# Performance work log

Measured on AMD Instinct MI355X. Metric: run time of the kernel, lower is better.

Reference implementation:

```python
import jax, jax.numpy as jnp
import numpy as np

B, L, R = 4, 2048, 1024        # batch, seq_len, residual_dim
HID, EXP, K = 64, 2, 3          # hidden_dim, expansion_factor, conv_kernel_size
D = HID * EXP                   # ssm_input_dim = 128
N = HID                         # SSM state size = 64


def setup_inputs() -> dict:
    key = jax.random.key(0)
    ks = jax.random.split(key, 16)
    g = lambda k, s: jax.random.normal(k, s, dtype=jnp.float32) * 0.02
    inp = {
        "up_x":   jax.random.normal(ks[0], (B, L, R), dtype=jnp.float32),
        "W_up":   g(ks[1], (R, 2 * D)),
        "b_up":   g(ks[2], (2 * D,)),
        "conv_w": g(ks[3], (D, K)),          # depthwise Conv1d weight [C,1,K] squeezed
        "conv_b": g(ks[4], (D,)),
        "W_delta": g(ks[5], (D, D)),
        "b_delta": g(ks[6], (D,)),
        "W_B":    g(ks[7], (D, N)),
        "b_B":    g(ks[8], (N,)),
        "W_C":    g(ks[9], (D, N)),
        "b_C":    g(ks[10], (N,)),
        "A_log":  jnp.log(jnp.broadcast_to(jnp.arange(1, N + 1, dtype=jnp.float32), (D, N))),
        "D_skip": jnp.ones((D,), dtype=jnp.float32),
        "W_down": g(ks[11], (D, R)),
        "b_down": g(ks[12], (R,)),
    }
    return inp


def reference(up_x, W_up, b_up, conv_w, conv_b, W_delta, b_delta,
              W_B, b_B, W_C, b_C, A_log, D_skip, W_down, b_down):
    Lq = up_x.shape[1]
    u = up_x @ W_up + b_up                               # [B,L,2D]
    left, right = jnp.split(u, 2, axis=-1)               # each [B,L,D]

    # causal depthwise conv (pad left K-1, truncate to L)
    xp = jnp.pad(left, ((0, 0), (K - 1, 0), (0, 0)))     # [B,L+K-1,D]
    conv = sum(conv_w[:, k] * xp[:, k:k + Lq, :] for k in range(K)) + conv_b
    x = jax.nn.silu(conv)                                # [B,L,D]

    # S6 selective scan
    delta = jax.nn.softplus(x @ W_delta + b_delta)       # [B,L,D]
    Bm = x @ W_B + b_B                                   # [B,L,N]
    Cm = x @ W_C + b_C                                   # [B,L,N]
    A = -jnp.exp(A_log)                                  # [D,N]
    dA = jnp.exp(delta[..., None] * A)                   # [B,L,D,N]
    dBx = delta[..., None] * Bm[:, :, None, :] * x[..., None]  # [B,L,D,N]

    def step(h, inputs):
        dA_t, dBx_t, C_t = inputs                        # [B,D,N],[B,D,N],[B,N]
        h = dA_t * h + dBx_t
        y_t = jnp.einsum('bdn,bn->bd', h, C_t)
        return h, y_t

    h0 = jnp.zeros((up_x.shape[0], D, N), dtype=x.dtype)
    _, ys = jax.lax.scan(step, h0, (jnp.swapaxes(dA, 0, 1),
                                    jnp.swapaxes(dBx, 0, 1),
                                    jnp.swapaxes(Cm, 0, 1)))
    y = jnp.swapaxes(ys, 0, 1) + D_skip * x              # [B,L,D]

    gated = y * jax.nn.silu(right)                       # SiLU gate
    return gated @ W_down + b_down                       # [B,L,R]
```

## Files before the change

### kernel.cpp

```cpp
#include <hip/hip_runtime.h>
#include <math.h>

#define B_ 4
#define L_ 2048
#define R_ 1024
#define D_ 128
#define N_ 64
#define TWO_D 256
#define M_ (B_*L_)

#define LNC 5
#define NC 32

#define LSTR 68
#define LSTRX 136

typedef __attribute__((ext_vector_type(8))) short bf16x8;
typedef __attribute__((ext_vector_type(4))) float f32x4;
typedef __attribute__((ext_vector_type(4))) unsigned short u16x4;

__device__ __forceinline__ float silu_f(float z) {
    return z * __builtin_amdgcn_rcpf(1.0f + __expf(-z));
}

__device__ __forceinline__ float softplus_f(float z) {
    return fmaxf(z, 0.0f) + __logf(1.0f + __expf(-fabsf(z)));
}

__device__ __forceinline__ short f2bf(float f) {
    union { float f; unsigned int u; } v; v.f = f;
    unsigned int r = v.u + 0x7FFF + ((v.u >> 16) & 1);
    return (short)(r >> 16);
}

__device__ __forceinline__ float bf2f(unsigned short s) {
    union { float f; unsigned int u; } v;
    v.u = ((unsigned int)s) << 16;
    return v.f;
}

__device__ __forceinline__ bf16x8 pack8(float4 a, float4 b) {
    bf16x8 r;
    r[0] = f2bf(a.x); r[1] = f2bf(a.y); r[2] = f2bf(a.z); r[3] = f2bf(a.w);
    r[4] = f2bf(b.x); r[5] = f2bf(b.y); r[6] = f2bf(b.z); r[7] = f2bf(b.w);
    return r;
}

__global__ __launch_bounds__(256) void gemm_up_splitk(
    const float* __restrict__ A,
    const float* __restrict__ W,
    float* __restrict__ P0,
    float* __restrict__ P1)
{
    __shared__ short Al[128 * LSTR];
    __shared__ short Bl[64 * LSTR];

    int lid = blockIdx.x;
    int xcd = lid & 7;
    int slot = lid >> 3;
    int bm = xcd * 8 + (slot >> 3);
    int r3 = slot & 7;
    int bn = r3 & 3;
    int split = r3 >> 2;
    float* P = split ? P1 : P0;
    int k0 = split * 512;

    int tid = threadIdx.x;
    int w = tid >> 6, l = tid & 63;
    int lm = l & 15, q = l >> 4;
    int wm = w * 32;

    f32x4 acc[2][4];
    #pragma unroll
    for (int i = 0; i < 2; i++)
        #pragma unroll
        for (int f = 0; f < 4; f++)
            acc[i][f] = (f32x4){0.f, 0.f, 0.f, 0.f};

    int ar = tid >> 1, ak = (tid & 1) * 16;
    int bcol = tid & 63, bk = (tid >> 6) * 8;

    const float* Ag = A + (size_t)(bm * 128 + ar) * 1024 + k0 + ak;
    const float* Wg = W + (size_t)k0 * TWO_D + (size_t)bn * 64 + bcol;

    for (int kt = 0; kt < 512; kt += 32) {
        float4 a0 = *(const float4*)(Ag + kt);
        float4 a1 = *(const float4*)(Ag + kt + 4);
        float4 a2 = *(const float4*)(Ag + kt + 8);
        float4 a3 = *(const float4*)(Ag + kt + 12);
        *(bf16x8*)&Al[ar * LSTR + ak]     = pack8(a0, a1);
        *(bf16x8*)&Al[ar * LSTR + ak + 8] = pack8(a2, a3);

        float w0 = Wg[(size_t)(kt + bk + 0) * TWO_D];
        float w1 = Wg[(size_t)(kt + bk + 1) * TWO_D];
        float w2 = Wg[(size_t)(kt + bk + 2) * TWO_D];
        float w3 = Wg[(size_t)(kt + bk + 3) * TWO_D];
        float w4 = Wg[(size_t)(kt + bk + 4) * TWO_D];
        float w5 = Wg[(size_t)(kt + bk + 5) * TWO_D];
        float w6 = Wg[(size_t)(kt + bk + 6) * TWO_D];
        float w7 = Wg[(size_t)(kt + bk + 7) * TWO_D];
        *(bf16x8*)&Bl[bcol * LSTR + bk] =
            pack8(make_float4(w0, w1, w2, w3), make_float4(w4, w5, w6, w7));

        __syncthreads();

        bf16x8 af0 = *(bf16x8*)&Al[(wm + lm) * LSTR + q * 8];
        bf16x8 af1 = *(bf16x8*)&Al[(wm + 16 + lm) * LSTR + q * 8];
        bf16x8 bfr[4];
        #pragma unroll
        for (int f = 0; f < 4; f++)
            bfr[f] = *(bf16x8*)&Bl[(f * 16 + lm) * LSTR + q * 8];

        #pragma unroll
        for (int f = 0; f < 4; f++) {
            acc[0][f] = __builtin_amdgcn_mfma_f32_16x16x32_bf16(af0, bfr[f], acc[0][f], 0, 0, 0);
            acc[1][f] = __builtin_amdgcn_mfma_f32_16x16x32_bf16(af1, bfr[f], acc[1][f], 0, 0, 0);
        }

        __syncthreads();
    }

    #pragma unroll
    for (int i = 0; i < 2; i++)
        #pragma unroll
        for (int f = 0; f < 4; f++)
            #pragma unroll
            for (int e = 0; e < 4; e++) {
                int row = bm * 128 + wm + i * 16 + q * 4 + e;
                int col = bn * 64 + f * 16 + lm;
                P[(size_t)row * TWO_D + col] = acc[i][f][e];
            }
}

__global__ __launch_bounds__(256) void convproj_mfma(
    const float* __restrict__ P0,
    const float* __restrict__ P1,
    const float* __restrict__ b_up,
    const float* __restrict__ conv_w,
    const float* __restrict__ conv_b,
    const float* __restrict__ W_delta, const float* __restrict__ b_delta,
    const float* __restrict__ W_B,     const float* __restrict__ b_B,
    const float* __restrict__ W_C,     const float* __restrict__ b_C,
    unsigned short* __restrict__ x,
    float* __restrict__ u,
    unsigned short* __restrict__ delta,
    unsigned short* __restrict__ Bm,
    unsigned short* __restrict__ Cm)
{
    __shared__ float uu[66 * 128];
    __shared__ short Xl[64 * LSTRX];
    __shared__ short Bl[64 * LSTR];

    int lid = blockIdx.x;
    int xcd = lid & 7;
    int slot = lid >> 3;
    int bm = xcd * 16 + (slot >> 2);
    int bn = slot & 3;
    int tid = threadIdx.x;

    bool seq_start = (bm & 31) == 0;

    #pragma unroll
    for (int i = 0; i < 9; i++) {
        int fi = tid + i * 256;
        if (fi < 2112) {
            int row = fi >> 5;
            int c4 = (fi & 31) * 4;
            int gr = bm * 64 + row - 2;
            float4 v;
            if (seq_start && row < 2) {
                v = make_float4(0.f, 0.f, 0.f, 0.f);
            } else {
                size_t gi = (size_t)gr * TWO_D + c4;
                float4 p0 = *(const float4*)&P0[gi];
                float4 p1 = *(const float4*)&P1[gi];
                float4 bb = *(const float4*)&b_up[c4];
                v = make_float4(p0.x + p1.x + bb.x, p0.y + p1.y + bb.y,
                                p0.z + p1.z + bb.z, p0.w + p1.w + bb.w);
            }
            *(float4*)&uu[fi * 4] = v;
        }
    }

    if (bn == 1) {
        #pragma unroll
        for (int i = 0; i < 8; i++) {
            int fi = tid + i * 256;
            int row = fi >> 5;
            int c4 = (fi & 31) * 4 + 128;
            int gr = bm * 64 + row;
            size_t gi = (size_t)gr * TWO_D + c4;
            float4 p0 = *(const float4*)&P0[gi];
            float4 p1 = *(const float4*)&P1[gi];
            float4 bb = *(const float4*)&b_up[c4];
            *(float4*)&u[gi] = make_float4(p0.x + p1.x + bb.x, p0.y + p1.y + bb.y,
                                           p0.z + p1.z + bb.z, p0.w + p1.w + bb.w);
        }
    }
    __syncthreads();

    #pragma unroll
    for (int i = 0; i < 8; i++) {
        int fi = tid + i * 256;
        int row = fi >> 5;
        int c4 = (fi & 31) * 4;
        float4 v2 = *(const float4*)&uu[(row + 2) * 128 + c4];
        float4 v1 = *(const float4*)&uu[(row + 1) * 128 + c4];
        float4 v0 = *(const float4*)&uu[(row + 0) * 128 + c4];
        float4 z;
        {
            float w0 = conv_w[(c4 + 0) * 3 + 0], w1 = conv_w[(c4 + 0) * 3 + 1], w2 = conv_w[(c4 + 0) * 3 + 2];
            z.x = silu_f(fmaf(w0, v0.x, fmaf(w1, v1.x, fmaf(w2, v2.x, conv_b[c4 + 0]))));
        }
        {
            float w0 = conv_w[(c4 + 1) * 3 + 0], w1 = conv_w[(c4 + 1) * 3 + 1], w2 = conv_w[(c4 + 1) * 3 + 2];
            z.y = silu_f(fmaf(w0, v0.y, fmaf(w1, v1.y, fmaf(w2, v2.y, conv_b[c4 + 1]))));
        }
        {
            float w0 = conv_w[(c4 + 2) * 3 + 0], w1 = conv_w[(c4 + 2) * 3 + 1], w2 = conv_w[(c4 + 2) * 3 + 2];
            z.z = silu_f(fmaf(w0, v0.z, fmaf(w1, v1.z, fmaf(w2, v2.z, conv_b[c4 + 2]))));
        }
        {
            float w0 = conv_w[(c4 + 3) * 3 + 0], w1 = conv_w[(c4 + 3) * 3 + 1], w2 = conv_w[(c4 + 3) * 3 + 2];
            z.w = silu_f(fmaf(w0, v0.w, fmaf(w1, v1.w, fmaf(w2, v2.w, conv_b[c4 + 3]))));
        }
        short4 zb;
        zb.x = f2bf(z.x); zb.y = f2bf(z.y); zb.z = f2bf(z.z); zb.w = f2bf(z.w);
        *(short4*)&Xl[row * LSTRX + c4] = zb;
        if (bn == 0) {
            int gr = bm * 64 + row;
            *(short4*)&x[(size_t)gr * D_ + c4] = zb;
        }
    }

    const float* Wsel; const float* bsel; int wstride;
    if (bn < 2)       { Wsel = W_delta + bn * 64; bsel = b_delta + bn * 64; wstride = 128; }
    else if (bn == 2) { Wsel = W_B;               bsel = b_B;               wstride = 64;  }
    else              { Wsel = W_C;               bsel = b_C;               wstride = 64;  }

    int w = tid >> 6, l = tid & 63;
    int lm = l & 15, q = l >> 4;
    int wm = (w & 1) * 32, wn = (w >> 1) * 32;

    f32x4 acc00 = {0,0,0,0}, acc01 = {0,0,0,0}, acc10 = {0,0,0,0}, acc11 = {0,0,0,0};

    int bcol = tid & 63, bk = (tid >> 6) * 8;
    const float* Wg = Wsel + bcol;

    __syncthreads();

    for (int kt = 0; kt < 128; kt += 32) {
        float w0 = Wg[(size_t)(kt + bk + 0) * wstride];
        float w1 = Wg[(size_t)(kt + bk + 1) * wstride];
        float w2 = Wg[(size_t)(kt + bk + 2) * wstride];
        float w3 = Wg[(size_t)(kt + bk + 3) * wstride];
        float w4 = Wg[(size_t)(kt + bk + 4) * wstride];
        float w5 = Wg[(size_t)(kt + bk + 5) * wstride];
        float w6 = Wg[(size_t)(kt + bk + 6) * wstride];
        float w7 = Wg[(size_t)(kt + bk + 7) * wstride];
        *(bf16x8*)&Bl[bcol * LSTR + bk] =
            pack8(make_float4(w0, w1, w2, w3), make_float4(w4, w5, w6, w7));

        __syncthreads();

        bf16x8 af0 = *(bf16x8*)&Xl[(wm + lm) * LSTRX + kt + q * 8];
        bf16x8 af1 = *(bf16x8*)&Xl[(wm + 16 + lm) * LSTRX + kt + q * 8];
        bf16x8 bf0 = *(bf16x8*)&Bl[(wn + lm) * LSTR + q * 8];
        bf16x8 bf1 = *(bf16x8*)&Bl[(wn + 16 + lm) * LSTR + q * 8];

        acc00 = __builtin_amdgcn_mfma_f32_16x16x32_bf16(af0, bf0, acc00, 0, 0, 0);
        acc01 = __builtin_amdgcn_mfma_f32_16x16x32_bf16(af0, bf1, acc01, 0, 0, 0);
        acc10 = __builtin_amdgcn_mfma_f32_16x16x32_bf16(af1, bf0, acc10, 0, 0, 0);
        acc11 = __builtin_amdgcn_mfma_f32_16x16x32_bf16(af1, bf1, acc11, 0, 0, 0);

        __syncthreads();
    }

    #pragma unroll
    for (int i = 0; i < 4; i++) {
        int r0 = bm * 64 + wm + q * 4 + i;
        int r1 = r0 + 16;
        int c0 = wn + lm;
        int c1 = c0 + 16;
        float v00 = acc00[i] + bsel[c0];
        float v01 = acc01[i] + bsel[c1];
        float v10 = acc10[i] + bsel[c0];
        float v11 = acc11[i] + bsel[c1];
        if (bn < 2) {
            int cc0 = bn * 64 + c0, cc1 = bn * 64 + c1;
            delta[(size_t)r0 * D_ + cc0] = (unsigned short)f2bf(softplus_f(v00));
            delta[(size_t)r0 * D_ + cc1] = (unsigned short)f2bf(softplus_f(v01));
            delta[(size_t)r1 * D_ + cc0] = (unsigned short)f2bf(softplus_f(v10));
            delta[(size_t)r1 * D_ + cc1] = (unsigned short)f2bf(softplus_f(v11));
        } else if (bn == 2) {
            Bm[(size_t)r0 * N_ + c0] = (unsigned short)f2bf(v00);
            Bm[(size_t)r0 * N_ + c1] = (unsigned short)f2bf(v01);
            Bm[(size_t)r1 * N_ + c0] = (unsigned short)f2bf(v10);
            Bm[(size_t)r1 * N_ + c1] = (unsigned short)f2bf(v11);
        } else {
            Cm[(size_t)r0 * N_ + c0] = (unsigned short)f2bf(v00);
            Cm[(size_t)r0 * N_ + c1] = (unsigned short)f2bf(v01);
            Cm[(size_t)r1 * N_ + c0] = (unsigned short)f2bf(v10);
            Cm[(size_t)r1 * N_ + c1] = (unsigned short)f2bf(v11);
        }
    }
}

__global__ __launch_bounds__(256) void scan_sumA(
    const unsigned short* __restrict__ delta,
    const unsigned short* __restrict__ x,
    const unsigned short* __restrict__ Bm,
    const float* __restrict__ A_log,
    float* __restrict__ ch_aprod,
    float* __restrict__ ch_h)
{
    constexpr int TCt = L_ >> LNC;

    int blk = blockIdx.x;
    int c = blk & (NC - 1);
    int dqg = (blk >> LNC) & 7;
    int b = blk >> (LNC + 3);
    int wv = threadIdx.x >> 6;
    int l = threadIdx.x & 63;
    int g = l >> 4, j = l & 15;
    int dq = dqg * 4 + wv;
    int d = dq * 4 + g;

    const float LOG2E = 1.44269504089f;
    float4 Ar = *(const float4*)&A_log[d * N_ + j * 4];
    float Ai0 = -__expf(Ar.x) * LOG2E;
    float Ai1 = -__expf(Ar.y) * LOG2E;
    float Ai2 = -__expf(Ar.z) * LOG2E;
    float Ai3 = -__expf(Ar.w) * LOG2E;

    size_t row0 = (size_t)b * L_ + c * TCt;
    const unsigned short* dp = delta + row0 * D_ + d;
    const unsigned short* xp = x     + row0 * D_ + d;
    const unsigned short* bp = Bm    + row0 * N_ + j * 4;

    float h0 = 0, h1 = 0, h2 = 0, h3 = 0;
    float S = 0;

    #pragma unroll 8
    for (int t = 0; t < TCt; t++) {
        float dl = bf2f(dp[t * D_]);
        float xv = bf2f(xp[t * D_]);
        u16x4 bv = *(const u16x4*)&bp[t * N_];
        float e0 = exp2f(dl * Ai0);
        float e1 = exp2f(dl * Ai1);
        float e2 = exp2f(dl * Ai2);
        float e3 = exp2f(dl * Ai3);
        float dbx = dl * xv;
        h0 = fmaf(e0, h0, dbx * bf2f(bv[0]));
        h1 = fmaf(e1, h1, dbx * bf2f(bv[1]));
        h2 = fmaf(e2, h2, dbx * bf2f(bv[2]));
        h3 = fmaf(e3, h3, dbx * bf2f(bv[3]));
        S += dl;
    }

    size_t ci = (((size_t)b * D_ + d) * NC + c) * N_ + j * 4;
    *(float4*)&ch_aprod[ci] = make_float4(exp2f(Ai0 * S), exp2f(Ai1 * S),
                                          exp2f(Ai2 * S), exp2f(Ai3 * S));
    *(float4*)&ch_h[ci]     = make_float4(h0, h1, h2, h3);
}

__global__ __launch_bounds__(64) void scan_prefix(
    float* __restrict__ aprod_hin,
    const float* __restrict__ ch_h)
{
    int idx = blockIdx.x * 64 + threadIdx.x;
    int n = idx & 63;
    int rest = idx >> 6;
    size_t base = (size_t)rest * NC * N_ + n;
    float h = 0.0f;
    #pragma unroll 8
    for (int c = 0; c < NC; c++) {
        size_t o = base + (size_t)c * N_;
        float a  = aprod_hin[o];
        float hh = ch_h[o];
        aprod_hin[o] = h;
        h = fmaf(a, h, hh);
    }
}

__global__ __launch_bounds__(256) void scan_outB(
    const unsigned short* __restrict__ delta,
    const unsigned short* __restrict__ x,
    const unsigned short* __restrict__ Bm,
    const unsigned short* __restrict__ Cm,
    const float* __restrict__ A_log,
    const float* __restrict__ D_skip,
    const float* __restrict__ hin,
    const float* __restrict__ u,
    short* __restrict__ gated)
{
    constexpr int TCt = L_ >> LNC;
    __shared__ float yl[TCt * 16];

    int blk = blockIdx.x;
    int c = blk & (NC - 1);
    int dqg = (blk >> LNC) & 7;
    int b = blk >> (LNC + 3);
    int wv = threadIdx.x >> 6;
    int l = threadIdx.x & 63;
    int g = l >> 4, j = l & 15;
    int dq = dqg * 4 + wv;
    int d = dq * 4 + g;

    const float LOG2E = 1.44269504089f;
    float4 Ar = *(const float4*)&A_log[d * N_ + j * 4];
    float Ai0 = -__expf(Ar.x) * LOG2E;
    float Ai1 = -__expf(Ar.y) * LOG2E;
    float Ai2 = -__expf(Ar.z) * LOG2E;
    float Ai3 = -__expf(Ar.w) * LOG2E;
    float dsk = D_skip[d];

    float4 hv = *(const float4*)&hin[(((size_t)b * D_ + d) * NC + c) * N_ + j * 4];
    float h0 = hv.x, h1 = hv.y, h2 = hv.z, h3 = hv.w;

    size_t row0 = (size_t)b * L_ + c * TCt;
    const unsigned short* dp = delta + row0 * D_ + d;
    const unsigned short* xp = x     + row0 * D_ + d;
    const unsigned short* bp = Bm    + row0 * N_ + j * 4;
    const unsigned short* cp = Cm    + row0 * N_ + j * 4;

    #pragma unroll 8
    for (int t = 0; t < TCt; t++) {
        float dl = bf2f(dp[t * D_]);
        float xv = bf2f(xp[t * D_]);
        u16x4 bv = *(const u16x4*)&bp[t * N_];
        u16x4 cv = *(const u16x4*)&cp[t * N_];
        float e0 = exp2f(dl * Ai0);
        float e1 = exp2f(dl * Ai1);
        float e2 = exp2f(dl * Ai2);
        float e3 = exp2f(dl * Ai3);
        float dbx = dl * xv;
        h0 = fmaf(e0, h0, dbx * bf2f(bv[0]));
        h1 = fmaf(e1, h1, dbx * bf2f(bv[1]));
        h2 = fmaf(e2, h2, dbx * bf2f(bv[2]));
        h3 = fmaf(e3, h3, dbx * bf2f(bv[3]));
        float p = fmaf(h0, bf2f(cv[0]), fmaf(h1, bf2f(cv[1]),
                  fmaf(h2, bf2f(cv[2]), h3 * bf2f(cv[3]))));
        p += __shfl_xor(p, 1, 64);
        p += __shfl_xor(p, 2, 64);
        p += __shfl_xor(p, 4, 64);
        p += __shfl_xor(p, 8, 64);
        if (j == 0) yl[t * 16 + wv * 4 + g] = fmaf(dsk, xv, p);
    }

    __syncthreads();

    int tid = threadIdx.x;
    {
        int t = tid >> 2;
        int c4 = (tid & 3) * 4;
        size_t row = row0 + t;
        float4 yv = *(float4*)&yl[t * 16 + c4];
        float4 gv = *(const float4*)&u[row * TWO_D + 128 + dqg * 16 + c4];
        short4 o;
        o.x = f2bf(yv.x * silu_f(gv.x));
        o.y = f2bf(yv.y * silu_f(gv.y));
        o.z = f2bf(yv.z * silu_f(gv.z));
        o.w = f2bf(yv.w * silu_f(gv.w));
        *(short4*)&gated[row * D_ + dqg * 16 + c4] = o;
    }
}

__global__ __launch_bounds__(256) void gemm_down_mfma(
    const short* __restrict__ gated,
    const float* __restrict__ W,
    const float* __restrict__ bias,
    float* __restrict__ out)
{
    __shared__ short Al[64 * LSTR];
    __shared__ short Bl[64 * LSTR];

    int lid = blockIdx.x;
    int xcd = lid & 7;
    int slot = lid >> 3;
    int bm = xcd * 16 + (slot >> 4);
    int bn = slot & 15;

    int tid = threadIdx.x;
    int w = tid >> 6, l = tid & 63;
    int lm = l & 15, q = l >> 4;
    int wm = (w & 1) * 32, wn = (w >> 1) * 32;

    f32x4 acc00 = {0,0,0,0}, acc01 = {0,0,0,0}, acc10 = {0,0,0,0}, acc11 = {0,0,0,0};

    int ar = tid >> 2, ak = (tid & 3) * 8;
    int bcol = tid & 63, bk = (tid >> 6) * 8;

    const short* Gg = gated + (size_t)(bm * 64 + ar) * D_ + ak;
    const float* Wg = W + (size_t)bn * 64 + bcol;

    for (int kt = 0; kt < 128; kt += 32) {
        bf16x8 av = *(const bf16x8*)(Gg + kt);
        *(bf16x8*)&Al[ar * LSTR + ak] = av;

        float w0 = Wg[(size_t)(kt + bk + 0) * R_];
        float w1 = Wg[(size_t)(kt + bk + 1) * R_];
        float w2 = Wg[(size_t)(kt + bk + 2) * R_];
        float w3 = Wg[(size_t)(kt + bk + 3) * R_];
        float w4 = Wg[(size_t)(kt + bk + 4) * R_];
        float w5 = Wg[(size_t)(kt + bk + 5) * R_];
        float w6 = Wg[(size_t)(kt + bk + 6) * R_];
        float w7 = Wg[(size_t)(kt + bk + 7) * R_];
        *(bf16x8*)&Bl[bcol * LSTR + bk] =
            pack8(make_float4(w0, w1, w2, w3), make_float4(w4, w5, w6, w7));

        __syncthreads();

        bf16x8 af0 = *(bf16x8*)&Al[(wm + lm) * LSTR + q * 8];
        bf16x8 af1 = *(bf16x8*)&Al[(wm + 16 + lm) * LSTR + q * 8];
        bf16x8 bf0 = *(bf16x8*)&Bl[(wn + lm) * LSTR + q * 8];
        bf16x8 bf1 = *(bf16x8*)&Bl[(wn + 16 + lm) * LSTR + q * 8];

        acc00 = __builtin_amdgcn_mfma_f32_16x16x32_bf16(af0, bf0, acc00, 0, 0, 0);
        acc01 = __builtin_amdgcn_mfma_f32_16x16x32_bf16(af0, bf1, acc01, 0, 0, 0);
        acc10 = __builtin_amdgcn_mfma_f32_16x16x32_bf16(af1, bf0, acc10, 0, 0, 0);
        acc11 = __builtin_amdgcn_mfma_f32_16x16x32_bf16(af1, bf1, acc11, 0, 0, 0);

        __syncthreads();
    }

    #pragma unroll
    for (int i = 0; i < 4; i++) {
        int r0 = bm * 64 + wm + q * 4 + i;
        int r1 = r0 + 16;
        int c0 = bn * 64 + wn + lm;
        int c1 = c0 + 16;
        out[(size_t)r0 * R_ + c0] = acc00[i] + bias[c0];
        out[(size_t)r0 * R_ + c1] = acc01[i] + bias[c1];
        out[(size_t)r1 * R_ + c0] = acc10[i] + bias[c0];
        out[(size_t)r1 * R_ + c1] = acc11[i] + bias[c1];
    }
}

extern "C" void kernel_launch(void* const* d_in, const int* in_sizes, int n_in,
                              void* d_out, int out_size, void* d_ws, size_t ws_size,
                              hipStream_t stream)
{
    const float* up_x    = (const float*)d_in[0];
    const float* W_up    = (const float*)d_in[1];
    const float* b_up    = (const float*)d_in[2];
    const float* conv_w  = (const float*)d_in[3];
    const float* conv_b  = (const float*)d_in[4];
    const float* W_delta = (const float*)d_in[5];
    const float* b_delta = (const float*)d_in[6];
    const float* W_B     = (const float*)d_in[7];
    const float* b_B     = (const float*)d_in[8];
    const float* W_C     = (const float*)d_in[9];
    const float* b_C     = (const float*)d_in[10];
    const float* A_log   = (const float*)d_in[11];
    const float* D_skip  = (const float*)d_in[12];
    const float* W_down  = (const float*)d_in[13];
    const float* b_down  = (const float*)d_in[14];

    float* out = (float*)d_out;
    float* ws  = (float*)d_ws;

    float* u = ws;
    unsigned short* x16     = (unsigned short*)(u + (size_t)M_ * TWO_D);
    unsigned short* delta16 = x16     + (size_t)M_ * D_;
    unsigned short* Bm16    = delta16 + (size_t)M_ * D_;
    unsigned short* Cm16    = Bm16    + (size_t)M_ * N_;
    unsigned short* gated   = Cm16    + (size_t)M_ * N_;
    float* ch_aprod = (float*)(gated + (size_t)M_ * D_);
    float* ch_h     = ch_aprod + (size_t)B_ * D_ * NC * N_;
    float* P0       = ch_h     + (size_t)B_ * D_ * NC * N_;
    float* P1       = P0       + (size_t)M_ * TWO_D;

    gemm_up_splitk<<<512, 256, 0, stream>>>(up_x, W_up, P0, P1);

    convproj_mfma<<<512, 256, 0, stream>>>(
        P0, P1, b_up, conv_w, conv_b,
        W_delta, b_delta, W_B, b_B, W_C, b_C,
        x16, u, delta16, Bm16, Cm16);

    scan_sumA<<<(B_ * (D_ / 4) * NC) / 4, 256, 0, stream>>>(
        delta16, x16, Bm16, A_log, ch_aprod, ch_h);
    scan_prefix<<<(B_ * D_ * N_) / 64, 64, 0, stream>>>(
        ch_aprod, ch_h);
    scan_outB<<<(B_ * (D_ / 4) * NC) / 4, 256, 0, stream>>>(
        delta16, x16, Bm16, Cm16, A_log, D_skip, ch_aprod, u, (short*)gated);

    gemm_down_mfma<<<2048, 256, 0, stream>>>(
        (const short*)gated, W_down, b_down, out);
}
```

Measured before the change: 237.2 us.

## Stage scan chunk inputs in LDS and double the number of scan chunks

Both scan kernels now cooperatively preload each chunk's delta, x, B (and C) tiles into shared memory with vectorized coalesced loads, then run the recurrence from LDS instead of strided per-thread global loads. The chunk count is doubled so each block handles a shorter time slice, which raises parallelism and keeps the staged tiles small. In exchange, the prefix pass has twice as many chunks to combine and chunk-state buffers double. The epilogue is also restricted to the first 128 threads to match the shorter chunk.

Result: faster. 202.6 us (-14.6%).

```diff
diff --git a/kernel.cpp b/kernel.cpp
--- a/kernel.cpp
+++ b/kernel.cpp
@@ -9,8 +9,8 @@
 #define TWO_D 256
 #define M_ (B_*L_)
 
-#define LNC 5
-#define NC 32
+#define LNC 6
+#define NC 64
 
 #define LSTR 68
 #define LSTRX 136
@@ -315,16 +315,36 @@
     float* __restrict__ ch_h)
 {
     constexpr int TCt = L_ >> LNC;
+    __shared__ unsigned short ld_d[TCt * 16];
+    __shared__ unsigned short ld_x[TCt * 16];
+    __shared__ unsigned short ld_b[TCt * 64];
 
     int blk = blockIdx.x;
     int c = blk & (NC - 1);
     int dqg = (blk >> LNC) & 7;
     int b = blk >> (LNC + 3);
-    int wv = threadIdx.x >> 6;
-    int l = threadIdx.x & 63;
+    int tid = threadIdx.x;
+    int wv = tid >> 6;
+    int l = tid & 63;
     int g = l >> 4, j = l & 15;
-    int dq = dqg * 4 + wv;
-    int d = dq * 4 + g;
+    int d0 = dqg * 16;
+    int d = d0 + wv * 4 + g;
+    int dloc = wv * 4 + g;
+
+    size_t row0 = (size_t)b * L_ + c * TCt;
+
+    {
+        int t = (tid & 127) >> 2;
+        int c4 = (tid & 3) * 4;
+        const unsigned short* src = (tid < 128) ? delta : x;
+        unsigned short* dst = (tid < 128) ? ld_d : ld_x;
+        *(u16x4*)&dst[t * 16 + c4] = *(const u16x4*)&src[(row0 + t) * D_ + d0 + c4];
+    }
+    {
+        int t = tid >> 3;
+        int c8 = (tid & 7) * 8;
+        *(bf16x8*)&ld_b[t * 64 + c8] = *(const bf16x8*)&Bm[(row0 + t) * N_ + c8];
+    }
 
     const float LOG2E = 1.44269504089f;
     float4 Ar = *(const float4*)&A_log[d * N_ + j * 4];
@@ -333,19 +353,16 @@
     float Ai2 = -__expf(Ar.z) * LOG2E;
     float Ai3 = -__expf(Ar.w) * LOG2E;
 
-    size_t row0 = (size_t)b * L_ + c * TCt;
-    const unsigned short* dp = delta + row0 * D_ + d;
-    const unsigned short* xp = x     + row0 * D_ + d;
-    const unsigned short* bp = Bm    + row0 * N_ + j * 4;
+    __syncthreads();
 
     float h0 = 0, h1 = 0, h2 = 0, h3 = 0;
     float S = 0;
 
     #pragma unroll 8
     for (int t = 0; t < TCt; t++) {
-        float dl = bf2f(dp[t * D_]);
-        float xv = bf2f(xp[t * D_]);
-        u16x4 bv = *(const u16x4*)&bp[t * N_];
+        float dl = bf2f(ld_d[t * 16 + dloc]);
+        float xv = bf2f(ld_x[t * 16 + dloc]);
+        u16x4 bv = *(const u16x4*)&ld_b[t * 64 + j * 4];
         float e0 = exp2f(dl * Ai0);
         float e1 = exp2f(dl * Ai1);
         float e2 = exp2f(dl * Ai2);
@@ -395,17 +412,39 @@
     short* __restrict__ gated)
 {
     constexpr int TCt = L_ >> LNC;
+    __shared__ unsigned short ld_d[TCt * 16];
+    __shared__ unsigned short ld_x[TCt * 16];
+    __shared__ unsigned short ld_b[TCt * 64];
+    __shared__ unsigned short ld_c[TCt * 64];
     __shared__ float yl[TCt * 16];
 
     int blk = blockIdx.x;
     int c = blk & (NC - 1);
     int dqg = (blk >> LNC) & 7;
     int b = blk >> (LNC + 3);
-    int wv = threadIdx.x >> 6;
-    int l = threadIdx.x & 63;
+    int tid = threadIdx.x;
+    int wv = tid >> 6;
+    int l = tid & 63;
     int g = l >> 4, j = l & 15;
-    int dq = dqg * 4 + wv;
-    int d = dq * 4 + g;
+    int d0 = dqg * 16;
+    int d = d0 + wv * 4 + g;
+    int dloc = wv * 4 + g;
+
+    size_t row0 = (size_t)b * L_ + c * TCt;
+
+    {
+        int t = (tid & 127) >> 2;
+        int c4 = (tid & 3) * 4;
+        const unsigned short* src = (tid < 128) ? delta : x;
+        unsigned short* dst = (tid < 128) ? ld_d : ld_x;
+        *(u16x4*)&dst[t * 16 + c4] = *(const u16x4*)&src[(row0 + t) * D_ + d0 + c4];
+    }
+    {
+        int t = tid >> 3;
+        int c8 = (tid & 7) * 8;
+        *(bf16x8*)&ld_b[t * 64 + c8] = *(const bf16x8*)&Bm[(row0 + t) * N_ + c8];
+        *(bf16x8*)&ld_c[t * 64 + c8] = *(const bf16x8*)&Cm[(row0 + t) * N_ + c8];
+    }
 
     const float LOG2E = 1.44269504089f;
     float4 Ar = *(const float4*)&A_log[d * N_ + j * 4];
@@ -418,18 +457,14 @@
     float4 hv = *(const float4*)&hin[(((size_t)b * D_ + d) * NC + c) * N_ + j * 4];
     float h0 = hv.x, h1 = hv.y, h2 = hv.z, h3 = hv.w;
 
-    size_t row0 = (size_t)b * L_ + c * TCt;
-    const unsigned short* dp = delta + row0 * D_ + d;
-    const unsigned short* xp = x     + row0 * D_ + d;
-    const unsigned short* bp = Bm    + row0 * N_ + j * 4;
-    const unsigned short* cp = Cm    + row0 * N_ + j * 4;
+    __syncthreads();
 
     #pragma unroll 8
     for (int t = 0; t < TCt; t++) {
-        float dl = bf2f(dp[t * D_]);
-        float xv = bf2f(xp[t * D_]);
-        u16x4 bv = *(const u16x4*)&bp[t * N_];
-        u16x4 cv = *(const u16x4*)&cp[t * N_];
+        float dl = bf2f(ld_d[t * 16 + dloc]);
+        float xv = bf2f(ld_x[t * 16 + dloc]);
+        u16x4 bv = *(const u16x4*)&ld_b[t * 64 + j * 4];
+        u16x4 cv = *(const u16x4*)&ld_c[t * 64 + j * 4];
         float e0 = exp2f(dl * Ai0);
         float e1 = exp2f(dl * Ai1);
         float e2 = exp2f(dl * Ai2);
@@ -445,24 +480,23 @@
         p += __shfl_xor(p, 2, 64);
         p += __shfl_xor(p, 4, 64);
         p += __shfl_xor(p, 8, 64);
-        if (j == 0) yl[t * 16 + wv * 4 + g] = fmaf(dsk, xv, p);
+        if (j == 0) yl[t * 16 + dloc] = fmaf(dsk, xv, p);
     }
 
     __syncthreads();
 
-    int tid = threadIdx.x;
-    {
+    if (tid < 128) {
         int t = tid >> 2;
         int c4 = (tid & 3) * 4;
         size_t row = row0 + t;
         float4 yv = *(float4*)&yl[t * 16 + c4];
-        float4 gv = *(const float4*)&u[row * TWO_D + 128 + dqg * 16 + c4];
+        float4 gv = *(const float4*)&u[row * TWO_D + 128 + d0 + c4];
         short4 o;
         o.x = f2bf(yv.x * silu_f(gv.x));
         o.y = f2bf(yv.y * silu_f(gv.y));
         o.z = f2bf(yv.z * silu_f(gv.z));
         o.w = f2bf(yv.w * silu_f(gv.w));
-        *(short4*)&gated[row * D_ + dqg * 16 + c4] = o;
+        *(short4*)&gated[row * D_ + d0 + c4] = o;
     }
 }
 
@@ -578,11 +612,11 @@
         W_delta, b_delta, W_B, b_B, W_C, b_C,
         x16, u, delta16, Bm16, Cm16);
 
-    scan_sumA<<<(B_ * (D_ / 4) * NC) / 4, 256, 0, stream>>>(
+    scan_sumA<<<B_ * 8 * NC, 256, 0, stream>>>(
         delta16, x16, Bm16, A_log, ch_aprod, ch_h);
     scan_prefix<<<(B_ * D_ * N_) / 64, 64, 0, stream>>>(
         ch_aprod, ch_h);
-    scan_outB<<<(B_ * (D_ / 4) * NC) / 4, 256, 0, stream>>>(
+    scan_outB<<<B_ * 8 * NC, 256, 0, stream>>>(
         delta16, x16, Bm16, Cm16, A_log, D_skip, ch_aprod, u, (short*)gated);
 
     gemm_down_mfma<<<2048, 256, 0, stream>>>(
```
